# Performance work log

Measured on AMD Instinct MI355X. Metric: run time of the kernel, lower is better.

The kernel has to match this reference:

```python
import jax, jax.numpy as jnp
import numpy as np
from jax import lax

B, N, C, DFF, K = 32, 256, 256, 1024, 8
GRID = 128          # fixed jit-safe eta-phi grid (TF computes it dynamically via reduce_max)
GSIZE = 0.1         # grid_size init kwarg
LN_EPS = 1e-6
BN_EPS = 1e-3       # keras BatchNormalization default epsilon


def setup_inputs() -> dict:
    key = jax.random.key(0)
    ks = jax.random.split(key, 8)
    d = {}
    d['x'] = jax.random.normal(ks[0], (B, N, C), jnp.float32)
    d['coords'] = jax.random.normal(ks[1], (B, N, 2), jnp.float32)
    d['dw_kernel'] = jax.random.normal(ks[2], (K, K, 1, C), jnp.float32) * (1.0 / K)
    d['dw_bias'] = jnp.zeros((C,), jnp.float32)
    d['pw_w'] = jax.random.normal(ks[3], (C, C), jnp.float32) * (1.0 / np.sqrt(C))
    d['pw_b'] = jnp.zeros((C,), jnp.float32)
    d['ln_g'] = jnp.ones((C,), jnp.float32)
    d['ln_b'] = jnp.zeros((C,), jnp.float32)
    d['gi_w1'] = jax.random.normal(ks[4], (C, C), jnp.float32) * (1.0 / np.sqrt(C))
    d['gi_b1'] = jnp.zeros((C,), jnp.float32)
    d['gi_w2'] = jax.random.normal(ks[5], (C, C), jnp.float32) * (1.0 / np.sqrt(C))
    d['gi_b2'] = jnp.zeros((C,), jnp.float32)
    for i in range(3):
        d[f'bn{i}_g'] = jnp.ones((C,), jnp.float32)
        d[f'bn{i}_b'] = jnp.zeros((C,), jnp.float32)
        d[f'bn{i}_m'] = jnp.zeros((C,), jnp.float32)
        d[f'bn{i}_v'] = jnp.ones((C,), jnp.float32)
    d['w_ff1'] = jax.random.normal(ks[6], (C, DFF), jnp.float32) * (1.0 / np.sqrt(C))
    d['b_ff1'] = jnp.zeros((DFF,), jnp.float32)
    d['w_ff2'] = jax.random.normal(ks[7], (DFF, C), jnp.float32) * (1.0 / np.sqrt(DFF))
    d['b_ff2'] = jnp.zeros((C,), jnp.float32)
    return d


def _bn_inf(x, g, b, m, v):
    # keras BatchNormalization, inference path, per-channel (last axis)
    return (x - m) * lax.rsqrt(v + BN_EPS) * g + b


def _layernorm(x, g, b):
    mu = jnp.mean(x, axis=-1, keepdims=True)
    var = jnp.mean(jnp.square(x - mu), axis=-1, keepdims=True)
    return (x - mu) * lax.rsqrt(var + LN_EPS) * g + b


def _forward(x, coords, dw_kernel, dw_bias, pw_w, pw_b, ln_g, ln_b,
             gi_w1, gi_b1, gi_w2, gi_b2,
             bn0_g, bn0_b, bn0_m, bn0_v,
             bn1_g, bn1_b, bn1_m, bn1_v,
             w_ff1, b_ff1, w_ff2, b_ff2,
             bn2_g, bn2_b, bn2_m, bn2_v):
    eta, phi = coords[..., 0], coords[..., 1]

    # ---- GeometricCPE ----
    residual = x
    eta_min = jnp.min(eta, axis=1, keepdims=True)
    phi_min = jnp.min(phi, axis=1, keepdims=True)
    ge = jnp.clip(((eta - eta_min) / GSIZE).astype(jnp.int32), 0, GRID - 1)  # [B,N]
    gp = jnp.clip(((phi - phi_min) / GSIZE).astype(jnp.int32), 0, GRID - 1)
    b_idx = jnp.arange(B)[:, None]                                           # [B,1]

    # scatter-add points into dense grid (tf.scatter_nd sums duplicates)
    grid = jnp.zeros((B, GRID, GRID, C), x.dtype).at[b_idx, ge, gp].add(x)

    # depthwise conv2d, SAME padding (even kernel: lo=3, hi=4 matches TF)
    grid = lax.conv_general_dilated(
        grid, dw_kernel, window_strides=(1, 1), padding='SAME',
        dimension_numbers=('NHWC', 'HWIO', 'NHWC'), feature_group_count=C)
    grid = grid + dw_bias

    out = grid[b_idx, ge, gp]                    # gather back, [B,N,C]
    out = out @ pw_w + pw_b                      # pointwise Dense
    out = _layernorm(out, ln_g, ln_b)
    x = residual + out

    # ---- GlobalInteractionLayer ----
    gctx = jnp.mean(x, axis=1)                   # [B,C]
    y = (gctx @ gi_w1 + gi_b1)[:, None, :] + (x @ gi_w2 + gi_b2)
    y = _bn_inf(y, bn0_g, bn0_b, bn0_m, bn0_v)

    x = _bn_inf(x + y, bn1_g, bn1_b, bn1_m, bn1_v)

    # ---- FFN ----
    y = jax.nn.relu(x @ w_ff1 + b_ff1) @ w_ff2 + b_ff2
    x = _bn_inf(x + y, bn2_g, bn2_b, bn2_m, bn2_v)
    return x


def reference(x, coords, dw_kernel, dw_bias, pw_w, pw_b, ln_g, ln_b,
              gi_w1, gi_b1, gi_w2, gi_b2,
              bn0_g, bn0_b, bn0_m, bn0_v,
              bn1_g, bn1_b, bn1_m, bn1_v,
              w_ff1, b_ff1, w_ff2, b_ff2,
              bn2_g, bn2_b, bn2_m, bn2_v):
    out = _forward(x, coords, dw_kernel, dw_bias, pw_w, pw_b, ln_g, ln_b,
                   gi_w1, gi_b1, gi_w2, gi_b2,
                   bn0_g, bn0_b, bn0_m, bn0_v,
                   bn1_g, bn1_b, bn1_m, bn1_v,
                   w_ff1, b_ff1, w_ff2, b_ff2,
                   bn2_g, bn2_b, bn2_m, bn2_v)
    return (out, coords)
```

## Files before the change

### kernel.cpp

```cpp
#include <hip/hip_runtime.h>
#include <cstdint>
#include <cstddef>

#define B_   32
#define N_   256
#define C_   256
#define DFF_ 1024

typedef unsigned short ushort_t;
typedef __attribute__((ext_vector_type(8))) short bf16x8;
typedef __attribute__((ext_vector_type(4))) float f32x4;

__device__ __forceinline__ ushort_t f2bf(float f) {
    unsigned u = __builtin_bit_cast(unsigned, f);
    u += 0x7FFFu + ((u >> 16) & 1u);
    return (ushort_t)(u >> 16);
}
__device__ __forceinline__ float bf2f(ushort_t b) {
    return __builtin_bit_cast(float, (unsigned)b << 16);
}

__device__ __forceinline__ unsigned swz64(unsigned a) {
    return a ^ (((a >> 7) & 7u) << 4);
}

#define GLL(src, dst) __builtin_amdgcn_global_load_lds( \
    (const __attribute__((address_space(1))) void*)(src), \
    (__attribute__((address_space(3))) void*)(dst), 16, 0, 0)

__global__ void k_prep(const float* __restrict__ coords,
                       ushort_t* __restrict__ nbr, int* __restrict__ ncnt,
                       const float* g0, const float* b0, const float* m0, const float* v0,
                       const float* g1, const float* b1, const float* m1, const float* v1,
                       const float* g2, const float* b2, const float* m2, const float* v2,
                       float* __restrict__ sh, float* __restrict__ coords_out,
                       const float* __restrict__ pw, const float* __restrict__ gi,
                       const float* __restrict__ ff1, const float* __restrict__ ff2,
                       ushort_t* __restrict__ tpw, ushort_t* __restrict__ tgi,
                       ushort_t* __restrict__ tff1, ushort_t* __restrict__ tff2) {
    int bid = blockIdx.x;
    if (bid < B_) {
        int b = bid, n = threadIdx.x;
        __shared__ float se[N_], sp[N_];
        __shared__ int sge[N_], sgp[N_];
        float eta = coords[(b * N_ + n) * 2 + 0];
        float phi = coords[(b * N_ + n) * 2 + 1];
        coords_out[b * 512 + n] = coords[b * 512 + n];
        coords_out[b * 512 + 256 + n] = coords[b * 512 + 256 + n];
        se[n] = eta; sp[n] = phi;
        __syncthreads();
        for (int s = 128; s > 0; s >>= 1) {
            if (n < s) {
                se[n] = fminf(se[n], se[n + s]);
                sp[n] = fminf(sp[n], sp[n + s]);
            }
            __syncthreads();
        }
        float emin = se[0], pmin = sp[0];
        int gi2 = (int)((eta - emin) / 0.1f); gi2 = gi2 < 0 ? 0 : (gi2 > 127 ? 127 : gi2);
        int pi = (int)((phi - pmin) / 0.1f); pi = pi < 0 ? 0 : (pi > 127 ? 127 : pi);
        sge[n] = gi2; sgp[n] = pi;
        __syncthreads();
        int cnt = 0;
        ushort_t* out = nbr + ((size_t)b * N_ + n) * N_;
        for (int m = 0; m < N_; ++m) {
            int dh = sge[m] - gi2 + 3;
            int dv = sgp[m] - pi + 3;
            if (((unsigned)dh < 8u) && ((unsigned)dv < 8u))
                out[cnt++] = (ushort_t)(m | ((dh * 8 + dv) << 8));
        }
        ncnt[b * N_ + n] = cnt;
    } else if (bid == B_) {
        int c = threadIdx.x;
        float s;
        s = g0[c] * rsqrtf(v0[c] + 1e-3f); sh[c]        = s; sh[256 + c]  = b0[c] - m0[c] * s;
        s = g1[c] * rsqrtf(v1[c] + 1e-3f); sh[512 + c]  = s; sh[768 + c]  = b1[c] - m1[c] * s;
        s = g2[c] * rsqrtf(v2[c] + 1e-3f); sh[1024 + c] = s; sh[1280 + c] = b2[c] - m2[c] * s;
    } else {
        __shared__ float s[32][33];
        int t2 = bid - (B_ + 1);
        const float* W; ushort_t* T; int K, Nn, t;
        if (t2 < 64)       { W = pw;  T = tpw;  K = 256;  Nn = 256;  t = t2; }
        else if (t2 < 128) { W = gi;  T = tgi;  K = 256;  Nn = 256;  t = t2 - 64; }
        else if (t2 < 384) { W = ff1; T = tff1; K = 256;  Nn = 1024; t = t2 - 128; }
        else               { W = ff2; T = tff2; K = 1024; Nn = 256;  t = t2 - 384; }
        int ntiles_n = Nn >> 5;
        int n0 = (t % ntiles_n) << 5, k0 = (t / ntiles_n) << 5;
        int tx = threadIdx.x & 31, ty = threadIdx.x >> 5;
        #pragma unroll
        for (int j = 0; j < 4; ++j)
            s[ty + j * 8][tx] = W[(size_t)(k0 + ty + j * 8) * Nn + n0 + tx];
        __syncthreads();
        #pragma unroll
        for (int j = 0; j < 4; ++j)
            T[(size_t)(n0 + ty + j * 8) * K + k0 + tx] = f2bf(s[tx][ty + j * 8]);
    }
}

__global__ __launch_bounds__(256) void k_cpe2(
        const float* __restrict__ x,
        const ushort_t* __restrict__ nbr, const int* __restrict__ ncnt,
        const float* __restrict__ dwk, const float* __restrict__ dwb,
        ushort_t* __restrict__ t0) {
    int wv = threadIdx.x >> 6, lane = threadIdx.x & 63;
    int bn = blockIdx.x * 4 + wv;
    int b = bn >> 8;
    int c0 = lane * 4;
    int cnt = ncnt[bn];
    const ushort_t* lst = nbr + (size_t)bn * N_;
    const float* xb = x + (size_t)b * N_ * C_;
    float4 a0 = *(const float4*)(dwb + c0);
    float4 a1 = {0.f, 0.f, 0.f, 0.f};
    float4 a2 = {0.f, 0.f, 0.f, 0.f};
    float4 a3 = {0.f, 0.f, 0.f, 0.f};
    int i = 0;
    for (; i + 4 <= cnt; i += 4) {
        int pk0 = lst[i], pk1 = lst[i + 1], pk2 = lst[i + 2], pk3 = lst[i + 3];
        float4 w0 = *(const float4*)(dwk + (pk0 >> 8) * C_ + c0);
        float4 v0 = *(const float4*)(xb + (pk0 & 255) * C_ + c0);
        float4 w1 = *(const float4*)(dwk + (pk1 >> 8) * C_ + c0);
        float4 v1 = *(const float4*)(xb + (pk1 & 255) * C_ + c0);
        float4 w2 = *(const float4*)(dwk + (pk2 >> 8) * C_ + c0);
        float4 v2 = *(const float4*)(xb + (pk2 & 255) * C_ + c0);
        float4 w3 = *(const float4*)(dwk + (pk3 >> 8) * C_ + c0);
        float4 v3 = *(const float4*)(xb + (pk3 & 255) * C_ + c0);
        a0.x = fmaf(w0.x, v0.x, a0.x); a0.y = fmaf(w0.y, v0.y, a0.y);
        a0.z = fmaf(w0.z, v0.z, a0.z); a0.w = fmaf(w0.w, v0.w, a0.w);
        a1.x = fmaf(w1.x, v1.x, a1.x); a1.y = fmaf(w1.y, v1.y, a1.y);
        a1.z = fmaf(w1.z, v1.z, a1.z); a1.w = fmaf(w1.w, v1.w, a1.w);
        a2.x = fmaf(w2.x, v2.x, a2.x); a2.y = fmaf(w2.y, v2.y, a2.y);
        a2.z = fmaf(w2.z, v2.z, a2.z); a2.w = fmaf(w2.w, v2.w, a2.w);
        a3.x = fmaf(w3.x, v3.x, a3.x); a3.y = fmaf(w3.y, v3.y, a3.y);
        a3.z = fmaf(w3.z, v3.z, a3.z); a3.w = fmaf(w3.w, v3.w, a3.w);
    }
    for (; i < cnt; ++i) {
        int pk = lst[i];
        float4 w = *(const float4*)(dwk + (pk >> 8) * C_ + c0);
        float4 v = *(const float4*)(xb + (pk & 255) * C_ + c0);
        a0.x = fmaf(w.x, v.x, a0.x); a0.y = fmaf(w.y, v.y, a0.y);
        a0.z = fmaf(w.z, v.z, a0.z); a0.w = fmaf(w.w, v.w, a0.w);
    }
    a0.x += a1.x + a2.x + a3.x;
    a0.y += a1.y + a2.y + a3.y;
    a0.z += a1.z + a2.z + a3.z;
    a0.w += a1.w + a2.w + a3.w;
    ushort4 ob; ob.x = f2bf(a0.x); ob.y = f2bf(a0.y); ob.z = f2bf(a0.z); ob.w = f2bf(a0.w);
    *(ushort4*)(t0 + (size_t)bn * C_ + c0) = ob;
}

template <int EPI>
__global__ __launch_bounds__(512) void k_gemmrow8(
    const ushort_t* __restrict__ A, const ushort_t* __restrict__ Wt,
    const float* __restrict__ bias,
    ushort_t* __restrict__ Cb,
    const float* __restrict__ residf, const ushort_t* __restrict__ residb,
    const float* __restrict__ p0, const float* __restrict__ p1,
    const float* __restrict__ p2, const float* __restrict__ p3,
    float* __restrict__ partial, const float* __restrict__ w1,
    const float* __restrict__ b1) {
    const int K = 256;
    __shared__ __align__(16) ushort_t sA[8192];
    __shared__ __align__(16) ushort_t sB[2][16384];
    __shared__ float red[8][32][2];
    __shared__ float sg[C_];
    __shared__ float sgp[2][C_];
    __shared__ float sgv[C_];
    int tid = threadIdx.x, lane = tid & 63, wv = tid >> 6;
    int rowBase = blockIdx.x * 32;
    int l16 = lane & 15, g = (lane >> 4) & 3;

    const ushort_t* aSrc[2];
    unsigned aOff[2];
    #pragma unroll
    for (int q = 0; q < 2; ++q) {
        unsigned P = q * 8192u + (unsigned)tid * 16u;
        unsigned L = swz64(P);
        unsigned chunk = L >> 12;
        unsigned row = (L >> 7) & 31u;
        unsigned k = (L & 127u) >> 1;
        aSrc[q] = A + (size_t)(rowBase + row) * K + chunk * 64 + k;
        aOff[q] = q * 8192u + (unsigned)wv * 1024u;
    }
    const ushort_t* bSrc[4];
    unsigned bOff[4];
    #pragma unroll
    for (int q = 0; q < 4; ++q) {
        unsigned P = q * 8192u + (unsigned)tid * 16u;
        unsigned L = swz64(P);
        bSrc[q] = Wt + (size_t)(L >> 7) * K + ((L & 127u) >> 1);
        bOff[q] = q * 8192u + (unsigned)wv * 1024u;
    }
    #pragma unroll
    for (int q = 0; q < 2; ++q) GLL(aSrc[q], (char*)sA + aOff[q]);
    #pragma unroll
    for (int q = 0; q < 4; ++q) GLL(bSrc[q], (char*)sB[0] + bOff[q]);

    if constexpr (EPI == 2) {
        int j = tid & 255, h = tid >> 8;
        if (h == 0) {
            int pb = (blockIdx.x >> 3) << 3;
            float s = 0.f;
            #pragma unroll
            for (int k2 = 0; k2 < 8; ++k2) s += partial[(size_t)(pb + k2) * C_ + j];
            sg[j] = s * (1.f / 256.f);
        }
        __syncthreads();
        float a2 = 0.f;
        #pragma unroll 8
        for (int c2 = h * 128; c2 < h * 128 + 128; ++c2)
            a2 = fmaf(sg[c2], w1[c2 * C_ + j], a2);
        sgp[h][j] = a2;
        __syncthreads();
        if (h == 0) sgv[j] = b1[j] + sgp[0][j] + sgp[1][j];
        __syncthreads();
    }

    unsigned oA[2][2], oB[2][2];
    #pragma unroll
    for (int mi = 0; mi < 2; ++mi)
        #pragma unroll
        for (int kk = 0; kk < 2; ++kk)
            oA[mi][kk] = swz64((unsigned)(((mi * 16 + l16) << 7) + (kk << 6) + (g << 4)));
    #pragma unroll
    for (int ni = 0; ni < 2; ++ni)
        #pragma unroll
        for (int kk = 0; kk < 2; ++kk)
            oB[ni][kk] = swz64((unsigned)(((wv * 32 + ni * 16 + l16) << 7) + (kk << 6) + (g << 4)));

    f32x4 acc[2][2] = {};
    int cur = 0;
    for (int t = 0; t < 4; ++t) {
        if (t < 3) {
            int o = (t + 1) << 6;
            #pragma unroll
            for (int q = 0; q < 4; ++q) GLL(bSrc[q] + o, (char*)sB[cur ^ 1] + bOff[q]);
            asm volatile("s_waitcnt vmcnt(4)" ::: "memory");
        } else {
            asm volatile("s_waitcnt vmcnt(0)" ::: "memory");
        }
        asm volatile("s_barrier" ::: "memory");
        const char* cA = (const char*)sA + t * 4096;
        const char* cB = (const char*)sB[cur];
        #pragma unroll
        for (int kk = 0; kk < 2; ++kk) {
            bf16x8 a0v = *(const bf16x8*)(cA + oA[0][kk]);
            bf16x8 a1v = *(const bf16x8*)(cA + oA[1][kk]);
            bf16x8 b0v = *(const bf16x8*)(cB + oB[0][kk]);
            bf16x8 b1v = *(const bf16x8*)(cB + oB[1][kk]);
            acc[0][0] = __builtin_amdgcn_mfma_f32_16x16x32_bf16(a0v, b0v, acc[0][0], 0, 0, 0);
            acc[0][1] = __builtin_amdgcn_mfma_f32_16x16x32_bf16(a0v, b1v, acc[0][1], 0, 0, 0);
            acc[1][0] = __builtin_amdgcn_mfma_f32_16x16x32_bf16(a1v, b0v, acc[1][0], 0, 0, 0);
            acc[1][1] = __builtin_amdgcn_mfma_f32_16x16x32_bf16(a1v, b1v, acc[1][1], 0, 0, 0);
        }
        asm volatile("s_barrier" ::: "memory");
        cur ^= 1;
    }

    float bv[2];
    #pragma unroll
    for (int ni = 0; ni < 2; ++ni) bv[ni] = bias[wv * 32 + ni * 16 + l16];
    #pragma unroll
    for (int mi = 0; mi < 2; ++mi)
        #pragma unroll
        for (int ni = 0; ni < 2; ++ni)
            #pragma unroll
            for (int j = 0; j < 4; ++j)
                acc[mi][ni][j] += bv[ni];

    if constexpr (EPI == 4) {
        #pragma unroll
        for (int mi = 0; mi < 2; ++mi)
            #pragma unroll
            for (int j = 0; j < 4; ++j) {
                float s = acc[mi][0][j] + acc[mi][1][j];
                float q = acc[mi][0][j] * acc[mi][0][j] + acc[mi][1][j] * acc[mi][1][j];
                #pragma unroll
                for (int off = 1; off < 16; off <<= 1) {
                    s += __shfl_xor(s, off);
                    q += __shfl_xor(q, off);
                }
                if (l16 == 0) {
                    int r = mi * 16 + g * 4 + j;
                    red[wv][r][0] = s;
                    red[wv][r][1] = q;
                }
            }
        __syncthreads();
        float colsum[2] = {0.f, 0.f};
        #pragma unroll
        for (int mi = 0; mi < 2; ++mi)
            #pragma unroll
            for (int j = 0; j < 4; ++j) {
                int r = mi * 16 + g * 4 + j;
                float sum = 0.f, sq = 0.f;
                #pragma unroll
                for (int w = 0; w < 8; ++w) { sum += red[w][r][0]; sq += red[w][r][1]; }
                float mu = sum * (1.f / 256.f);
                float var = fmaxf(sq * (1.f / 256.f) - mu * mu, 0.f);
                float rs = rsqrtf(var + 1e-6f);
                int row = rowBase + r;
                #pragma unroll
                for (int ni = 0; ni < 2; ++ni) {
                    int col = wv * 32 + ni * 16 + l16;
                    size_t idx = (size_t)row * C_ + col;
                    float o = residf[idx] + (acc[mi][ni][j] - mu) * rs * p0[col] + p1[col];
                    Cb[idx] = f2bf(o);
                    colsum[ni] += o;
                }
            }
        #pragma unroll
        for (int ni = 0; ni < 2; ++ni) {
            float s = colsum[ni];
            s += __shfl_xor(s, 16);
            s += __shfl_xor(s, 32);
            if (g == 0) partial[(size_t)blockIdx.x * C_ + wv * 32 + ni * 16 + l16] = s;
        }
    } else {
        #pragma unroll
        for (int ni = 0; ni < 2; ++ni) {
            int col = wv * 32 + ni * 16 + l16;
            float bvv = bv[ni];
            float gv = sgv[col];
            float s0v = p0[col], h0v = p1[col], s1v = p2[col], h1v = p3[col];
            #pragma unroll
            for (int mi = 0; mi < 2; ++mi)
                #pragma unroll
                for (int j = 0; j < 4; ++j) {
                    int row = rowBase + mi * 16 + g * 4 + j;
                    size_t idx = (size_t)row * C_ + col;
                    float v = acc[mi][ni][j] + gv;
                    v = v * s0v + h0v;
                    float o = (bf2f(residb[idx]) + v) * s1v + h1v;
                    Cb[idx] = f2bf(o);
                }
        }
    }
}

template <int EPI, int BN>
__global__ __launch_bounds__(256) void k_gemm128(
    const ushort_t* __restrict__ A, const ushort_t* __restrict__ Wt,
    const float* __restrict__ bias, int K, int Nn,
    ushort_t* __restrict__ Cb, float* __restrict__ Cf,
    const ushort_t* __restrict__ residb,
    const float* __restrict__ p0, const float* __restrict__ p1) {
    const int NI = BN / 32;
    const int QB = BN / 32;
    __shared__ __align__(16) ushort_t sA[2][8192];
    __shared__ __align__(16) ushort_t sB[2][BN * 64];
    int tid = threadIdx.x;
    int lane = tid & 63, wv = tid >> 6;
    int rowBase = blockIdx.y * 128, colBase = blockIdx.x * BN;
    int l16 = lane & 15, g = (lane >> 4) & 3;
    int wr = (wv >> 1) * 64, wc = (wv & 1) * (BN / 2);

    const ushort_t* aSrc[4];
    #pragma unroll
    for (int q = 0; q < 4; ++q) {
        unsigned P = q * 4096u + (unsigned)tid * 16;
        unsigned L = swz64(P);
        aSrc[q] = A + (size_t)(rowBase + (L >> 7)) * K + ((L >> 1) & 63u);
    }
    const ushort_t* bSrc[QB];
    #pragma unroll
    for (int q = 0; q < QB; ++q) {
        unsigned P = q * 4096u + (unsigned)tid * 16;
        unsigned L = swz64(P);
        bSrc[q] = Wt + (size_t)(colBase + (L >> 7)) * K + ((L >> 1) & 63u);
    }
    unsigned wb = (unsigned)(tid >> 6) * 1024;

    unsigned oA[4][2], oB[NI][2];
    #pragma unroll
    for (int mi = 0; mi < 4; ++mi)
        #pragma unroll
        for (int kk = 0; kk < 2; ++kk)
            oA[mi][kk] = swz64((unsigned)(((wr + mi * 16 + l16) << 7) + (kk << 6) + (g << 4)));
    #pragma unroll
    for (int ni = 0; ni < NI; ++ni)
        #pragma unroll
        for (int kk = 0; kk < 2; ++kk)
            oB[ni][kk] = swz64((unsigned)(((wc + ni * 16 + l16) << 7) + (kk << 6) + (g << 4)));

    f32x4 acc[4][NI] = {};
    int nt = K >> 6;

    #pragma unroll
    for (int q = 0; q < 4; ++q) GLL(aSrc[q], (char*)sA[0] + q * 4096 + wb);
    #pragma unroll
    for (int q = 0; q < QB; ++q) GLL(bSrc[q], (char*)sB[0] + q * 4096 + wb);

    int cur = 0;
    for (int t = 0; t < nt; ++t) {
        if (t + 1 < nt) {
            int o = (t + 1) << 6;
            #pragma unroll
            for (int q = 0; q < 4; ++q) GLL(aSrc[q] + o, (char*)sA[cur ^ 1] + q * 4096 + wb);
            #pragma unroll
            for (int q = 0; q < QB; ++q) GLL(bSrc[q] + o, (char*)sB[cur ^ 1] + q * 4096 + wb);
            if constexpr (BN == 128) asm volatile("s_waitcnt vmcnt(8)" ::: "memory");
            else                     asm volatile("s_waitcnt vmcnt(6)" ::: "memory");
        } else {
            asm volatile("s_waitcnt vmcnt(0)" ::: "memory");
        }
        asm volatile("s_barrier" ::: "memory");
        const char* cA = (const char*)sA[cur];
        const char* cB = (const char*)sB[cur];
        #pragma unroll
        for (int kk = 0; kk < 2; ++kk) {
            bf16x8 af[4], bff[NI];
            #pragma unroll
            for (int mi = 0; mi < 4; ++mi) af[mi] = *(const bf16x8*)(cA + oA[mi][kk]);
            #pragma unroll
            for (int ni = 0; ni < NI; ++ni) bff[ni] = *(const bf16x8*)(cB + oB[ni][kk]);
            #pragma unroll
            for (int mi = 0; mi < 4; ++mi)
                #pragma unroll
                for (int ni = 0; ni < NI; ++ni)
                    acc[mi][ni] = __builtin_amdgcn_mfma_f32_16x16x32_bf16(af[mi], bff[ni], acc[mi][ni], 0, 0, 0);
        }
        asm volatile("s_barrier" ::: "memory");
        cur ^= 1;
    }

    #pragma unroll
    for (int ni = 0; ni < NI; ++ni) {
        int col = colBase + wc + ni * 16 + l16;
        float bvv = bias[col];
        float s0v = 0.f, h0v = 0.f;
        if constexpr (EPI == 3) { s0v = p0[col]; h0v = p1[col]; }
        #pragma unroll
        for (int mi = 0; mi < 4; ++mi)
            #pragma unroll
            for (int j = 0; j < 4; ++j) {
                int row = rowBase + wr + mi * 16 + g * 4 + j;
                size_t idx = (size_t)row * Nn + col;
                float v = acc[mi][ni][j] + bvv;
                if constexpr (EPI == 1) {
                    Cb[idx] = f2bf(fmaxf(v, 0.f));
                } else {
                    Cf[idx] = (bf2f(residb[idx]) + v) * s0v + h0v;
                }
            }
    }
}

extern "C" void kernel_launch(void* const* d_in, const int* in_sizes, int n_in,
                              void* d_out, int out_size, void* d_ws, size_t ws_size,
                              hipStream_t stream) {
    const float* x      = (const float*)d_in[0];
    const float* coords = (const float*)d_in[1];
    const float* dwk    = (const float*)d_in[2];
    const float* dwb    = (const float*)d_in[3];
    const float* pw_w   = (const float*)d_in[4];
    const float* pw_b   = (const float*)d_in[5];
    const float* ln_g   = (const float*)d_in[6];
    const float* ln_b   = (const float*)d_in[7];
    const float* gi_w1  = (const float*)d_in[8];
    const float* gi_b1  = (const float*)d_in[9];
    const float* gi_w2  = (const float*)d_in[10];
    const float* gi_b2  = (const float*)d_in[11];
    const float* bn0g = (const float*)d_in[12], *bn0b = (const float*)d_in[13];
    const float* bn0m = (const float*)d_in[14], *bn0v = (const float*)d_in[15];
    const float* bn1g = (const float*)d_in[16], *bn1b = (const float*)d_in[17];
    const float* bn1m = (const float*)d_in[18], *bn1v = (const float*)d_in[19];
    const float* bn2g = (const float*)d_in[20], *bn2b = (const float*)d_in[21];
    const float* bn2m = (const float*)d_in[22], *bn2v = (const float*)d_in[23];
    const float* w_ff1 = (const float*)d_in[24];
    const float* b_ff1 = (const float*)d_in[25];
    const float* w_ff2 = (const float*)d_in[26];
    const float* b_ff2 = (const float*)d_in[27];

    char* ws = (char*)d_ws;
    int*      ncnt    = (int*)(ws + 0);
    float*    bnsh    = (float*)(ws + 32768);
    float*    partial = (float*)(ws + 40960);
    ushort_t* WtPW    = (ushort_t*)(ws + 303104);
    ushort_t* WtGI    = (ushort_t*)(ws + 434176);
    ushort_t* WtF1    = (ushort_t*)(ws + 565248);
    ushort_t* WtF2    = (ushort_t*)(ws + 1089536);
    ushort_t* nbr     = (ushort_t*)(ws + 1613824);
    ushort_t* x1b     = (ushort_t*)(ws + 5808128);
    ushort_t* x2b     = (ushort_t*)(ws + 10002432);
    ushort_t* t0      = (ushort_t*)(ws + 14196736);
    ushort_t* u_b     = (ushort_t*)(ws + 18391040);
    float*    outx    = (float*)d_out;

    const int M = B_ * N_;

    k_prep<<<B_ + 1 + 640, 256, 0, stream>>>(
        coords, nbr, ncnt,
        bn0g, bn0b, bn0m, bn0v, bn1g, bn1b, bn1m, bn1v, bn2g, bn2b, bn2m, bn2v,
        bnsh, outx + (size_t)M * C_,
        pw_w, gi_w2, w_ff1, w_ff2, WtPW, WtGI, WtF1, WtF2);

    k_cpe2<<<M / 4, 256, 0, stream>>>(x, nbr, ncnt, dwk, dwb, t0);

    k_gemmrow8<4><<<M / 32, 512, 0, stream>>>(
        t0, WtPW, pw_b, x1b, x, nullptr,
        ln_g, ln_b, nullptr, nullptr,
        partial, nullptr, nullptr);

    k_gemmrow8<2><<<M / 32, 512, 0, stream>>>(
        x1b, WtGI, gi_b2, x2b, nullptr, x1b,
        bnsh, bnsh + 256, bnsh + 512, bnsh + 768,
        partial, gi_w1, gi_b1);

    k_gemm128<1, 128><<<dim3(DFF_ / 128, M / 128), 256, 0, stream>>>(
        x2b, WtF1, b_ff1, C_, DFF_, u_b, nullptr, nullptr, nullptr, nullptr);

    k_gemm128<3, 64><<<dim3(C_ / 64, M / 128), 256, 0, stream>>>(
        u_b, WtF2, b_ff2, DFF_, C_, nullptr, outx, x2b,
        bnsh + 1024, bnsh + 1280);
}
```

Baseline: 94.97 us.

## Fuse pointwise+LN and global-interaction GEMMs into one kernel with per-batch spin barrier

Merges the two row-block GEMM kernels into a single kernel. The LayerNorm residual output stays in shared memory as bf16 instead of going through a global x1b buffer, and the per-batch mean is synchronised through an atomic counter spin-wait across the 8 blocks of each batch. The FFN GEMM grids are also transposed so row tiles vary fastest, which changes the order in which tiles are scheduled. This saves one launch and one global round trip, but the inter-block spin relies on all 8 blocks of a batch being co-resident, and it adds a memset launch.

```diff
diff --git a/kernel.cpp b/kernel.cpp
--- a/kernel.cpp
+++ b/kernel.cpp
@@ -148,16 +148,14 @@
     *(ushort4*)(t0 + (size_t)bn * C_ + c0) = ob;
 }
 
-template <int EPI>
-__global__ __launch_bounds__(512) void k_gemmrow8(
-    const ushort_t* __restrict__ A, const ushort_t* __restrict__ Wt,
-    const float* __restrict__ bias,
-    ushort_t* __restrict__ Cb,
-    const float* __restrict__ residf, const ushort_t* __restrict__ residb,
-    const float* __restrict__ p0, const float* __restrict__ p1,
-    const float* __restrict__ p2, const float* __restrict__ p3,
-    float* __restrict__ partial, const float* __restrict__ w1,
-    const float* __restrict__ b1) {
+__global__ __launch_bounds__(512) void k_mid(
+    const ushort_t* __restrict__ A, const ushort_t* __restrict__ WtPW,
+    const float* __restrict__ pwb, const float* __restrict__ x,
+    const float* __restrict__ ln_g, const float* __restrict__ ln_b,
+    float* __restrict__ partial, int* __restrict__ bcnt,
+    const ushort_t* __restrict__ WtGI, const float* __restrict__ gib2,
+    const float* __restrict__ w1, const float* __restrict__ b1,
+    const float* __restrict__ bnsh, ushort_t* __restrict__ x2b) {
     const int K = 256;
     __shared__ __align__(16) ushort_t sA[8192];
     __shared__ __align__(16) ushort_t sB[2][16384];
@@ -167,6 +165,7 @@
     __shared__ float sgv[C_];
     int tid = threadIdx.x, lane = tid & 63, wv = tid >> 6;
     int rowBase = blockIdx.x * 32;
+    int batch = blockIdx.x >> 3;
     int l16 = lane & 15, g = (lane >> 4) & 3;
 
     const ushort_t* aSrc[2];
@@ -175,33 +174,150 @@
     for (int q = 0; q < 2; ++q) {
         unsigned P = q * 8192u + (unsigned)tid * 16u;
         unsigned L = swz64(P);
-        unsigned chunk = L >> 12;
-        unsigned row = (L >> 7) & 31u;
-        unsigned k = (L & 127u) >> 1;
-        aSrc[q] = A + (size_t)(rowBase + row) * K + chunk * 64 + k;
+        aSrc[q] = A + (size_t)(rowBase + ((L >> 7) & 31u)) * K + (L >> 12) * 64u + ((L & 127u) >> 1);
         aOff[q] = q * 8192u + (unsigned)wv * 1024u;
     }
-    const ushort_t* bSrc[4];
-    unsigned bOff[4];
+    unsigned bRow[4], bKk[4], bOff[4];
     #pragma unroll
     for (int q = 0; q < 4; ++q) {
         unsigned P = q * 8192u + (unsigned)tid * 16u;
         unsigned L = swz64(P);
-        bSrc[q] = Wt + (size_t)(L >> 7) * K + ((L & 127u) >> 1);
+        bRow[q] = L >> 7;
+        bKk[q] = (L & 127u) >> 1;
         bOff[q] = q * 8192u + (unsigned)wv * 1024u;
     }
     #pragma unroll
     for (int q = 0; q < 2; ++q) GLL(aSrc[q], (char*)sA + aOff[q]);
     #pragma unroll
-    for (int q = 0; q < 4; ++q) GLL(bSrc[q], (char*)sB[0] + bOff[q]);
-
-    if constexpr (EPI == 2) {
+    for (int q = 0; q < 4; ++q)
+        GLL(WtPW + (size_t)bRow[q] * K + bKk[q], (char*)sB[0] + bOff[q]);
+
+    unsigned oA[2][2], oB[2][2];
+    #pragma unroll
+    for (int mi = 0; mi < 2; ++mi)
+        #pragma unroll
+        for (int kk = 0; kk < 2; ++kk)
+            oA[mi][kk] = swz64((unsigned)(((mi * 16 + l16) << 7) + (kk << 6) + (g << 4)));
+    #pragma unroll
+    for (int ni = 0; ni < 2; ++ni)
+        #pragma unroll
+        for (int kk = 0; kk < 2; ++kk)
+            oB[ni][kk] = swz64((unsigned)(((wv * 32 + ni * 16 + l16) << 7) + (kk << 6) + (g << 4)));
+
+    f32x4 acc[2][2] = {};
+    int cur = 0;
+    for (int t = 0; t < 4; ++t) {
+        if (t < 3) {
+            int o = (t + 1) << 6;
+            #pragma unroll
+            for (int q = 0; q < 4; ++q)
+                GLL(WtPW + (size_t)bRow[q] * K + o + bKk[q], (char*)sB[cur ^ 1] + bOff[q]);
+            asm volatile("s_waitcnt vmcnt(4)" ::: "memory");
+        } else {
+            asm volatile("s_waitcnt vmcnt(0)" ::: "memory");
+        }
+        asm volatile("s_barrier" ::: "memory");
+        const char* cA = (const char*)sA + t * 4096;
+        const char* cB = (const char*)sB[cur];
+        #pragma unroll
+        for (int kk = 0; kk < 2; ++kk) {
+            bf16x8 a0v = *(const bf16x8*)(cA + oA[0][kk]);
+            bf16x8 a1v = *(const bf16x8*)(cA + oA[1][kk]);
+            bf16x8 b0v = *(const bf16x8*)(cB + oB[0][kk]);
+            bf16x8 b1v = *(const bf16x8*)(cB + oB[1][kk]);
+            acc[0][0] = __builtin_amdgcn_mfma_f32_16x16x32_bf16(a0v, b0v, acc[0][0], 0, 0, 0);
+            acc[0][1] = __builtin_amdgcn_mfma_f32_16x16x32_bf16(a0v, b1v, acc[0][1], 0, 0, 0);
+            acc[1][0] = __builtin_amdgcn_mfma_f32_16x16x32_bf16(a1v, b0v, acc[1][0], 0, 0, 0);
+            acc[1][1] = __builtin_amdgcn_mfma_f32_16x16x32_bf16(a1v, b1v, acc[1][1], 0, 0, 0);
+        }
+        asm volatile("s_barrier" ::: "memory");
+        cur ^= 1;
+    }
+
+    #pragma unroll
+    for (int q = 0; q < 4; ++q)
+        GLL(WtGI + (size_t)bRow[q] * K + bKk[q], (char*)sB[0] + bOff[q]);
+
+    float bv[2];
+    #pragma unroll
+    for (int ni = 0; ni < 2; ++ni) bv[ni] = pwb[wv * 32 + ni * 16 + l16];
+    #pragma unroll
+    for (int mi = 0; mi < 2; ++mi)
+        #pragma unroll
+        for (int ni = 0; ni < 2; ++ni)
+            #pragma unroll
+            for (int j = 0; j < 4; ++j)
+                acc[mi][ni][j] += bv[ni];
+
+    #pragma unroll
+    for (int mi = 0; mi < 2; ++mi)
+        #pragma unroll
+        for (int j = 0; j < 4; ++j) {
+            float s = acc[mi][0][j] + acc[mi][1][j];
+            float q = acc[mi][0][j] * acc[mi][0][j] + acc[mi][1][j] * acc[mi][1][j];
+            #pragma unroll
+            for (int off = 1; off < 16; off <<= 1) {
+                s += __shfl_xor(s, off);
+                q += __shfl_xor(q, off);
+            }
+            if (l16 == 0) {
+                int r = mi * 16 + g * 4 + j;
+                red[wv][r][0] = s;
+                red[wv][r][1] = q;
+            }
+        }
+    __syncthreads();
+    float colsum[2] = {0.f, 0.f};
+    #pragma unroll
+    for (int mi = 0; mi < 2; ++mi)
+        #pragma unroll
+        for (int j = 0; j < 4; ++j) {
+            int r = mi * 16 + g * 4 + j;
+            float sum = 0.f, sq = 0.f;
+            #pragma unroll
+            for (int w = 0; w < 8; ++w) { sum += red[w][r][0]; sq += red[w][r][1]; }
+            float mu = sum * (1.f / 256.f);
+            float var = fmaxf(sq * (1.f / 256.f) - mu * mu, 0.f);
+            float rs = rsqrtf(var + 1e-6f);
+            int row = rowBase + r;
+            #pragma unroll
+            for (int ni = 0; ni < 2; ++ni) {
+                int col = wv * 32 + ni * 16 + l16;
+                float o = x[(size_t)row * C_ + col]
+                          + (acc[mi][ni][j] - mu) * rs * ln_g[col] + ln_b[col];
+                unsigned off = ((unsigned)col >> 6) * 4096u
+                               + swz64(((unsigned)r << 7) + (((unsigned)col & 63u) << 1));
+                *(ushort_t*)((char*)sA + off) = f2bf(o);
+                colsum[ni] += o;
+            }
+        }
+    #pragma unroll
+    for (int ni = 0; ni < 2; ++ni) {
+        float s = colsum[ni];
+        s += __shfl_xor(s, 16);
+        s += __shfl_xor(s, 32);
+        if (g == 0)
+            __hip_atomic_store(&partial[(size_t)blockIdx.x * C_ + wv * 32 + ni * 16 + l16],
+                               s, __ATOMIC_RELAXED, __HIP_MEMORY_SCOPE_AGENT);
+    }
+    __syncthreads();
+
+    if (tid == 0) {
+        __hip_atomic_fetch_add(&bcnt[batch], 1, __ATOMIC_RELEASE, __HIP_MEMORY_SCOPE_AGENT);
+        while (__hip_atomic_load(&bcnt[batch], __ATOMIC_ACQUIRE, __HIP_MEMORY_SCOPE_AGENT) < 8)
+            __builtin_amdgcn_s_sleep(2);
+    }
+    __syncthreads();
+
+    {
         int j = tid & 255, h = tid >> 8;
         if (h == 0) {
-            int pb = (blockIdx.x >> 3) << 3;
+            int pb = batch << 3;
             float s = 0.f;
             #pragma unroll
-            for (int k2 = 0; k2 < 8; ++k2) s += partial[(size_t)(pb + k2) * C_ + j];
+            for (int k2 = 0; k2 < 8; ++k2)
+                s += __hip_atomic_load(&partial[(size_t)(pb + k2) * C_ + j],
+                                       __ATOMIC_RELAXED, __HIP_MEMORY_SCOPE_AGENT);
             sg[j] = s * (1.f / 256.f);
         }
         __syncthreads();
@@ -215,25 +331,14 @@
         __syncthreads();
     }
 
-    unsigned oA[2][2], oB[2][2];
-    #pragma unroll
-    for (int mi = 0; mi < 2; ++mi)
-        #pragma unroll
-        for (int kk = 0; kk < 2; ++kk)
-            oA[mi][kk] = swz64((unsigned)(((mi * 16 + l16) << 7) + (kk << 6) + (g << 4)));
-    #pragma unroll
-    for (int ni = 0; ni < 2; ++ni)
-        #pragma unroll
-        for (int kk = 0; kk < 2; ++kk)
-            oB[ni][kk] = swz64((unsigned)(((wv * 32 + ni * 16 + l16) << 7) + (kk << 6) + (g << 4)));
-
-    f32x4 acc[2][2] = {};
-    int cur = 0;
+    f32x4 ac2[2][2] = {};
+    cur = 0;
     for (int t = 0; t < 4; ++t) {
         if (t < 3) {
             int o = (t + 1) << 6;
             #pragma unroll
-            for (int q = 0; q < 4; ++q) GLL(bSrc[q] + o, (char*)sB[cur ^ 1] + bOff[q]);
+            for (int q = 0; q < 4; ++q)
+                GLL(WtGI + (size_t)bRow[q] * K + o + bKk[q], (char*)sB[cur ^ 1] + bOff[q]);
             asm volatile("s_waitcnt vmcnt(4)" ::: "memory");
         } else {
             asm volatile("s_waitcnt vmcnt(0)" ::: "memory");
@@ -247,93 +352,35 @@
             bf16x8 a1v = *(const bf16x8*)(cA + oA[1][kk]);
             bf16x8 b0v = *(const bf16x8*)(cB + oB[0][kk]);
             bf16x8 b1v = *(const bf16x8*)(cB + oB[1][kk]);
-            acc[0][0] = __builtin_amdgcn_mfma_f32_16x16x32_bf16(a0v, b0v, acc[0][0], 0, 0, 0);
-            acc[0][1] = __builtin_amdgcn_mfma_f32_16x16x32_bf16(a0v, b1v, acc[0][1], 0, 0, 0);
-            acc[1][0] = __builtin_amdgcn_mfma_f32_16x16x32_bf16(a1v, b0v, acc[1][0], 0, 0, 0);
-            acc[1][1] = __builtin_amdgcn_mfma_f32_16x16x32_bf16(a1v, b1v, acc[1][1], 0, 0, 0);
+            ac2[0][0] = __builtin_amdgcn_mfma_f32_16x16x32_bf16(a0v, b0v, ac2[0][0], 0, 0, 0);
+            ac2[0][1] = __builtin_amdgcn_mfma_f32_16x16x32_bf16(a0v, b1v, ac2[0][1], 0, 0, 0);
+            ac2[1][0] = __builtin_amdgcn_mfma_f32_16x16x32_bf16(a1v, b0v, ac2[1][0], 0, 0, 0);
+            ac2[1][1] = __builtin_amdgcn_mfma_f32_16x16x32_bf16(a1v, b1v, ac2[1][1], 0, 0, 0);
         }
         asm volatile("s_barrier" ::: "memory");
         cur ^= 1;
     }
 
-    float bv[2];
-    #pragma unroll
-    for (int ni = 0; ni < 2; ++ni) bv[ni] = bias[wv * 32 + ni * 16 + l16];
-    #pragma unroll
-    for (int mi = 0; mi < 2; ++mi)
-        #pragma unroll
-        for (int ni = 0; ni < 2; ++ni)
-            #pragma unroll
-            for (int j = 0; j < 4; ++j)
-                acc[mi][ni][j] += bv[ni];
-
-    if constexpr (EPI == 4) {
-        #pragma unroll
-        for (int mi = 0; mi < 2; ++mi)
-            #pragma unroll
-            for (int j = 0; j < 4; ++j) {
-                float s = acc[mi][0][j] + acc[mi][1][j];
-                float q = acc[mi][0][j] * acc[mi][0][j] + acc[mi][1][j] * acc[mi][1][j];
-                #pragma unroll
-                for (int off = 1; off < 16; off <<= 1) {
-                    s += __shfl_xor(s, off);
-                    q += __shfl_xor(q, off);
-                }
-                if (l16 == 0) {
-                    int r = mi * 16 + g * 4 + j;
-                    red[wv][r][0] = s;
-                    red[wv][r][1] = q;
-                }
-            }
-        __syncthreads();
-        float colsum[2] = {0.f, 0.f};
+    const float* s0 = bnsh, *h0 = bnsh + 256, *s1 = bnsh + 512, *h1 = bnsh + 768;
+    #pragma unroll
+    for (int ni = 0; ni < 2; ++ni) {
+        int col = wv * 32 + ni * 16 + l16;
+        float bvv = gib2[col];
+        float gv = sgv[col];
+        float s0v = s0[col], h0v = h0[col], s1v = s1[col], h1v = h1[col];
         #pragma unroll
         for (int mi = 0; mi < 2; ++mi)
             #pragma unroll
             for (int j = 0; j < 4; ++j) {
                 int r = mi * 16 + g * 4 + j;
-                float sum = 0.f, sq = 0.f;
-                #pragma unroll
-                for (int w = 0; w < 8; ++w) { sum += red[w][r][0]; sq += red[w][r][1]; }
-                float mu = sum * (1.f / 256.f);
-                float var = fmaxf(sq * (1.f / 256.f) - mu * mu, 0.f);
-                float rs = rsqrtf(var + 1e-6f);
-                int row = rowBase + r;
-                #pragma unroll
-                for (int ni = 0; ni < 2; ++ni) {
-                    int col = wv * 32 + ni * 16 + l16;
-                    size_t idx = (size_t)row * C_ + col;
-                    float o = residf[idx] + (acc[mi][ni][j] - mu) * rs * p0[col] + p1[col];
-                    Cb[idx] = f2bf(o);
-                    colsum[ni] += o;
-                }
+                unsigned off = ((unsigned)col >> 6) * 4096u
+                               + swz64(((unsigned)r << 7) + (((unsigned)col & 63u) << 1));
+                float resid = bf2f(*(const ushort_t*)((const char*)sA + off));
+                float v = ac2[mi][ni][j] + bvv + gv;
+                v = v * s0v + h0v;
+                float o = (resid + v) * s1v + h1v;
+                x2b[(size_t)(rowBase + r) * C_ + col] = f2bf(o);
             }
-        #pragma unroll
-        for (int ni = 0; ni < 2; ++ni) {
-            float s = colsum[ni];
-            s += __shfl_xor(s, 16);
-            s += __shfl_xor(s, 32);
-            if (g == 0) partial[(size_t)blockIdx.x * C_ + wv * 32 + ni * 16 + l16] = s;
-        }
-    } else {
-        #pragma unroll
-        for (int ni = 0; ni < 2; ++ni) {
-            int col = wv * 32 + ni * 16 + l16;
-            float bvv = bv[ni];
-            float gv = sgv[col];
-            float s0v = p0[col], h0v = p1[col], s1v = p2[col], h1v = p3[col];
-            #pragma unroll
-            for (int mi = 0; mi < 2; ++mi)
-                #pragma unroll
-                for (int j = 0; j < 4; ++j) {
-                    int row = rowBase + mi * 16 + g * 4 + j;
-                    size_t idx = (size_t)row * C_ + col;
-                    float v = acc[mi][ni][j] + gv;
-                    v = v * s0v + h0v;
-                    float o = (bf2f(residb[idx]) + v) * s1v + h1v;
-                    Cb[idx] = f2bf(o);
-                }
-        }
     }
 }
 
@@ -350,7 +397,7 @@
     __shared__ __align__(16) ushort_t sB[2][BN * 64];
     int tid = threadIdx.x;
     int lane = tid & 63, wv = tid >> 6;
-    int rowBase = blockIdx.y * 128, colBase = blockIdx.x * BN;
+    int rowBase = blockIdx.x * 128, colBase = blockIdx.y * BN;
     int l16 = lane & 15, g = (lane >> 4) & 3;
     int wr = (wv >> 1) * 64, wc = (wv & 1) * (BN / 2);
 
@@ -474,19 +521,21 @@
     char* ws = (char*)d_ws;
     int*      ncnt    = (int*)(ws + 0);
     float*    bnsh    = (float*)(ws + 32768);
+    int*      bcnt    = (int*)(ws + 39936);
     float*    partial = (float*)(ws + 40960);
     ushort_t* WtPW    = (ushort_t*)(ws + 303104);
     ushort_t* WtGI    = (ushort_t*)(ws + 434176);
     ushort_t* WtF1    = (ushort_t*)(ws + 565248);
     ushort_t* WtF2    = (ushort_t*)(ws + 1089536);
     ushort_t* nbr     = (ushort_t*)(ws + 1613824);
-    ushort_t* x1b     = (ushort_t*)(ws + 5808128);
     ushort_t* x2b     = (ushort_t*)(ws + 10002432);
     ushort_t* t0      = (ushort_t*)(ws + 14196736);
     ushort_t* u_b     = (ushort_t*)(ws + 18391040);
     float*    outx    = (float*)d_out;
 
     const int M = B_ * N_;
+
+    hipMemsetAsync(bcnt, 0, B_ * sizeof(int), stream);
 
     k_prep<<<B_ + 1 + 640, 256, 0, stream>>>(
         coords, nbr, ncnt,
@@ -496,20 +545,14 @@
 
     k_cpe2<<<M / 4, 256, 0, stream>>>(x, nbr, ncnt, dwk, dwb, t0);
 
-    k_gemmrow8<4><<<M / 32, 512, 0, stream>>>(
-        t0, WtPW, pw_b, x1b, x, nullptr,
-        ln_g, ln_b, nullptr, nullptr,
-        partial, nullptr, nullptr);
-
-    k_gemmrow8<2><<<M / 32, 512, 0, stream>>>(
-        x1b, WtGI, gi_b2, x2b, nullptr, x1b,
-        bnsh, bnsh + 256, bnsh + 512, bnsh + 768,
-        partial, gi_w1, gi_b1);
-
-    k_gemm128<1, 128><<<dim3(DFF_ / 128, M / 128), 256, 0, stream>>>(
+    k_mid<<<M / 32, 512, 0, stream>>>(
+        t0, WtPW, pw_b, x, ln_g, ln_b, partial, bcnt,
+        WtGI, gi_b2, gi_w1, gi_b1, bnsh, x2b);
+
+    k_gemm128<1, 128><<<dim3(M / 128, DFF_ / 128), 256, 0, stream>>>(
         x2b, WtF1, b_ff1, C_, DFF_, u_b, nullptr, nullptr, nullptr, nullptr);
 
-    k_gemm128<3, 64><<<dim3(C_ / 64, M / 128), 256, 0, stream>>>(
+    k_gemm128<3, 64><<<dim3(M / 128, C_ / 64), 256, 0, stream>>>(
         u_b, WtF2, b_ff2, DFF_, C_, nullptr, outx, x2b,
         bnsh + 1024, bnsh + 1280);
 }
```

After: 101.7 us. 1.07x slower.
